# Kernel optimization log

Measured on AMD Instinct MI355X. Metric: run time of the kernel, lower is better.

## Reference

```python
import jax, jax.numpy as jnp
import numpy as np

N = 4096
DIN, DOUT, HID, CUTS = 16, 16, 16, 8
RADIUS = 9.0
SCALES = (1.0, 2.0, 3.0, 5.0, 10.0)
REG = 0.01
CHUNK = 512
GROUPS = 4
DINF = DIN + 2 * len(SCALES)  # 26


def leaky(v):
    return jnp.where(v >= 0, v, 0.2 * v)


def sqdist(a, b):
    d2 = jnp.sum(a * a, -1)[:, None] + jnp.sum(b * b, -1)[None, :] - 2.0 * (a @ b.T)
    return jnp.maximum(d2, 0.0)


def tangent_vectors(n):
    # Duff et al. branchless orthonormal basis, as in dMaSIF geometry_processing
    x, y, z = n[..., 0], n[..., 1], n[..., 2]
    s = jnp.where(z >= 0, 1.0, -1.0)
    a = -1.0 / (s + z)
    b = x * y * a
    t1 = jnp.stack([1.0 + s * x * x * a, s * b, -s * x], -1)
    t2 = jnp.stack([b, s + y * y * a, -y], -1)
    return jnp.stack([t1, t2], axis=-2)  # (..., 2, 3)


def group_norm(x, w, b, eps=1e-5):
    # torch GroupNorm(4, C) applied on (1, C, N): normalize over (C/G, N) per group
    n, c = x.shape
    xt = x.T.reshape(GROUPS, c // GROUPS, n)
    m = jnp.mean(xt, axis=(1, 2), keepdims=True)
    v = jnp.mean((xt - m) ** 2, axis=(1, 2), keepdims=True)
    xt = (xt - m) / jnp.sqrt(v + eps)
    return (xt.reshape(c, n) * w[:, None] + b[:, None]).T


def curvature_features(verts, normals):
    # dMaSIF curvatures(): per-scale Gaussian-window covariances, shape operator S = PPt^-1 PQt
    # Pairwise sums factorized into matmuls with the (N,N) window (no (N,N,8) intermediates).
    n_pts = verts.shape[0]
    d2 = sqdist(verts, verts)
    xx = (verts[:, :, None] * verts[:, None, :]).reshape(n_pts, 9)
    feats = []
    for s in SCALES:
        w = jnp.exp(-d2 / (2.0 * s * s))
        u_n = w @ normals  # scale-smoothed normals
        ns = u_n / jnp.maximum(jnp.linalg.norm(u_n, axis=-1, keepdims=True), 1e-12)
        uv = tangent_vectors(ns)  # (N,2,3)
        s0 = jnp.sum(w, 1)
        sx = w @ verts
        sn = w @ ns
        sxx = (w @ xx).reshape(n_pts, 3, 3)
        xn = (verts[:, :, None] * ns[:, None, :]).reshape(n_pts, 9)
        sxn = (w @ xn).reshape(n_pts, 3, 3)
        # sum_j w_ij (x_j-x_i)(x_j-x_i)^T  and  sum_j w_ij (x_j-x_i)(n_j-n_i)^T
        cxx = sxx - verts[:, :, None] * sx[:, None, :] - sx[:, :, None] * verts[:, None, :] \
              + s0[:, None, None] * verts[:, :, None] * verts[:, None, :]
        cxn = sxn - verts[:, :, None] * sn[:, None, :] - sx[:, :, None] * ns[:, None, :] \
              + s0[:, None, None] * verts[:, :, None] * ns[:, None, :]
        ppt = jnp.einsum('nka,nab,nlb->nkl', uv, cxx, uv) + REG * jnp.eye(2, dtype=verts.dtype)
        pqt = jnp.einsum('nka,nab,nlb->nkl', uv, cxn, uv)
        S = jnp.linalg.solve(ppt, pqt)  # (N,2,2)
        feats.append(jnp.clip(S[:, 0, 0] + S[:, 1, 1], -1.0, 1.0))            # mean curvature
        feats.append(jnp.clip(S[:, 0, 0] * S[:, 1, 1] - S[:, 0, 1] * S[:, 1, 0], -1.0, 1.0))  # gauss
    return jnp.stack(feats, -1)  # (N, 2*len(SCALES))


def _forward(verts, vnormals, x, os_w1, os_b1, os_w2, os_b2,
             ni_w1, ni_b1, ni_w2, ni_b2, gn_in_w, gn_in_b,
             cv_a1, cv_b1, cv_a2, cv_b2, no_w1, no_b1, no_w2, no_b2,
             gn_out_w, gn_out_b, ll_w1, ll_b1, ll_w2, ll_b2, lt_w, lt_b):
    curv = curvature_features(verts, vnormals)
    xf = jnp.concatenate([x, curv], axis=-1)  # (N, DINF)
    w = leaky(xf @ os_w1.T + os_b1) @ os_w2.T + os_b2  # orientation scores (N,1)

    # --- load_mesh: steer tangent frames along the gradient of w ---
    p = verts / RADIUS
    ndot = vnormals @ vnormals.T
    W = jnp.exp(-sqdist(p, p) * (2.0 - ndot) ** 2)  # pseudo-geodesic Gaussian window
    uv = tangent_vectors(vnormals)  # (N,2,3)
    ov3 = W @ (w * p) - (W @ w) * p  # sum_j W_ij w_j (x_j - x_i), factorized
    ov = jnp.einsum('nkd,nd->nk', uv, ov3) + 1e-5
    u = ov / jnp.sqrt(jnp.sum(ov * ov, -1, keepdims=True))
    ex, ey = u[:, 0:1], u[:, 1:2]
    u0, v0 = uv[:, 0], uv[:, 1]
    nuv = jnp.concatenate([vnormals[:, None, :],
                           (ex * u0 + ey * v0)[:, None, :],
                           (-ey * u0 + ex * v0)[:, None, :]], axis=1)  # (N,3,3)

    # --- dMaSIFConv layer ---
    h = leaky(leaky(xf @ ni_w1.T + ni_b1) @ ni_w2.T + ni_b2)
    h = group_norm(h, gn_in_w, gn_in_b)  # (N, HID)
    n_all = nuv[:, 0]
    nc = N // CHUNK
    pc = p.reshape(nc, CHUNK, 3)
    nuvc = nuv.reshape(nc, CHUNK, 3, 3)

    def block(args):
        pi, nuvi = args  # (C,3), (C,3,3)
        dx = p[None, :, :] - pi[:, None, :]  # (C,N,3)
        d2 = jnp.sum(dx * dx, -1)
        win = jnp.exp(-d2 * (2.0 - nuvi[:, 0] @ n_all.T) ** 2)  # (C,N)
        X = jnp.einsum('ckd,cnd->cnk', nuvi, dx)  # local coords (C,N,3)
        y = jax.nn.relu(X @ cv_a1.T + cv_b1) @ cv_a2.T + cv_b2  # filter MLP (C,N,HID)
        return jnp.einsum('cn,cnh,nh->ch', win, y, h)

    xi = jax.lax.map(jax.checkpoint(block), (pc, nuvc)).reshape(N, HID)
    xi = group_norm(leaky(leaky(xi @ no_w1.T + no_b1) @ no_w2.T + no_b2), gn_out_w, gn_out_b)
    xi = jax.nn.relu(xi @ ll_w1.T + ll_b1) @ ll_w2.T + ll_b2  # linear_layers[0]
    return xf @ lt_w.T + lt_b + xi  # linear_transform skip + conv branch


def setup_inputs():
    key = jax.random.key(0)
    ks = jax.random.split(key, 20)

    def lin(k, o, i):
        wk = jax.random.fold_in(k, 0)
        bk = jax.random.fold_in(k, 1)
        return ((1.0 / np.sqrt(i)) * jax.random.normal(wk, (o, i)),
                0.01 * jax.random.normal(bk, (o,)))

    verts = 10.0 * jax.random.normal(ks[0], (N, 3))
    vn = jax.random.normal(ks[1], (N, 3))
    vnormals = vn / jnp.linalg.norm(vn, axis=-1, keepdims=True)
    x = jax.random.normal(ks[2], (N, DIN))
    os_w1, os_b1 = lin(ks[3], DOUT, DINF)
    os_w2, os_b2 = lin(ks[4], 1, DOUT)
    ni_w1, ni_b1 = lin(ks[5], HID, DINF)
    ni_w2, ni_b2 = lin(ks[6], HID, HID)
    cv_a1 = jax.random.normal(ks[7], (CUTS, 3))
    cv_b1 = jax.random.uniform(ks[8], (CUTS,)) * 0.8 * jnp.sqrt(jnp.sum(cv_a1 ** 2, -1))
    cv_a2 = jax.random.uniform(ks[9], (HID, CUTS), minval=-1.0, maxval=1.0) / np.sqrt(CUTS)
    cv_b2 = jax.random.normal(ks[10], (HID,)) * 0.5 * jnp.sqrt(jnp.sum(cv_a2 ** 2, -1))
    no_w1, no_b1 = lin(ks[11], DOUT, HID)
    no_w2, no_b2 = lin(ks[12], DOUT, DOUT)
    ll_w1, ll_b1 = lin(ks[13], DOUT, DOUT)
    ll_w2, ll_b2 = lin(ks[14], DOUT, DOUT)
    lt_w, lt_b = lin(ks[15], DOUT, DINF)
    return {'verts': verts, 'vnormals': vnormals, 'x': x,
            'os_w1': os_w1, 'os_b1': os_b1, 'os_w2': os_w2, 'os_b2': os_b2,
            'ni_w1': ni_w1, 'ni_b1': ni_b1, 'ni_w2': ni_w2, 'ni_b2': ni_b2,
            'gn_in_w': jnp.ones(HID), 'gn_in_b': jnp.zeros(HID),
            'cv_a1': cv_a1, 'cv_b1': cv_b1, 'cv_a2': cv_a2, 'cv_b2': cv_b2,
            'no_w1': no_w1, 'no_b1': no_b1, 'no_w2': no_w2, 'no_b2': no_b2,
            'gn_out_w': jnp.ones(DOUT), 'gn_out_b': jnp.zeros(DOUT),
            'll_w1': ll_w1, 'll_b1': ll_b1, 'll_w2': ll_w2, 'll_b2': ll_b2,
            'lt_w': lt_w, 'lt_b': lt_b}


def reference(verts, vnormals, x, os_w1, os_b1, os_w2, os_b2,
              ni_w1, ni_b1, ni_w2, ni_b2, gn_in_w, gn_in_b,
              cv_a1, cv_b1, cv_a2, cv_b2, no_w1, no_b1, no_w2, no_b2,
              gn_out_w, gn_out_b, ll_w1, ll_b1, ll_w2, ll_b2, lt_w, lt_b):
    return _forward(verts, vnormals, x, os_w1, os_b1, os_w2, os_b2,
                    ni_w1, ni_b1, ni_w2, ni_b2, gn_in_w, gn_in_b,
                    cv_a1, cv_b1, cv_a2, cv_b2, no_w1, no_b1, no_w2, no_b2,
                    gn_out_w, gn_out_b, ll_w1, ll_b1, ll_w2, ll_b2, lt_w, lt_b)
```

## Files before the change

### kernel.cpp

```cpp
#include <hip/hip_runtime.h>
#include <hip/hip_bf16.h>
#include <math.h>

#define NPTS 4096
#define DINF 26
#define LOG2E 1.44269504088896f
#define JSPL 4

typedef float f32x4v __attribute__((ext_vector_type(4)));
typedef __bf16 bf16x8v __attribute__((ext_vector_type(8)));
typedef unsigned short ushort_t;

__device__ __forceinline__ float ldb(const float* p, int i){ return p[i]; }
__device__ __forceinline__ float lk(float v){ return v >= 0.0f ? v : 0.2f*v; }
__device__ __forceinline__ float wsum64(float v){
#pragma unroll
  for(int o=32;o>0;o>>=1) v += __shfl_down(v,o);
  return v;
}
__device__ __forceinline__ unsigned short f2bf(float f){
  return __builtin_bit_cast(unsigned short, __float2bfloat16(f));
}
__device__ __forceinline__ float bf2f(unsigned short u){
  return __bfloat162float(__builtin_bit_cast(__hip_bfloat16, u));
}
__device__ __forceinline__ void wave_lds_fence(){
  __builtin_amdgcn_wave_barrier();
  __builtin_amdgcn_s_waitcnt(0xC07F);
  __builtin_amdgcn_wave_barrier();
}
__device__ __forceinline__ void tangent(float nx,float ny,float nz,float* t1,float* t2){
  float s = (nz >= 0.0f) ? 1.0f : -1.0f;
  float a = -1.0f/(s+nz);
  float b = nx*ny*a;
  t1[0]=1.0f+s*nx*nx*a; t1[1]=s*b; t1[2]=-s*nx;
  t2[0]=b; t2[1]=s+ny*ny*a; t2[2]=-ny;
}

__global__ __launch_bounds__(256) void k0_convert(const float* __restrict__ verts,
                                                  const float* __restrict__ vnorm,
                                                  const float* __restrict__ x,
                                                  float* __restrict__ vertsF,
                                                  float* __restrict__ nF,
                                                  float* __restrict__ pF,
                                                  float* __restrict__ xfF){
  int i = blockIdx.x*blockDim.x + threadIdx.x;
  if(i >= NPTS) return;
#pragma unroll
  for(int d=0;d<3;d++){
    float v = verts[i*3+d];
    vertsF[i*3+d]=v;
    pF[i*3+d]=v*(1.0f/9.0f);
    nF[i*3+d]=vnorm[i*3+d];
  }
#pragma unroll
  for(int c=0;c<16;c++) xfF[i*DINF+c]=x[i*16+c];
}

__global__ __launch_bounds__(256) void kF(const float* __restrict__ vertsF,
                                          const float* __restrict__ nF,
                                          ushort_t* __restrict__ F1h,
                                          ushort_t* __restrict__ F1l){
  int j = blockIdx.x*256 + threadIdx.x;
  float vx=vertsF[j*3+0], vy=vertsF[j*3+1], vz=vertsF[j*3+2];
  float fv[16];
  fv[0]=1.0f; fv[1]=vx; fv[2]=vy; fv[3]=vz;
  fv[4]=vx*vx; fv[5]=vx*vy; fv[6]=vx*vz; fv[7]=vy*vy; fv[8]=vy*vz; fv[9]=vz*vz;
  fv[10]=nF[j*3+0]; fv[11]=nF[j*3+1]; fv[12]=nF[j*3+2];
  fv[13]=0.0f; fv[14]=0.0f; fv[15]=0.0f;
#pragma unroll
  for(int c=0;c<16;c++){
    unsigned short h=f2bf(fv[c]);
    F1h[c*NPTS+j]=h;
    F1l[c*NPTS+j]=f2bf(fv[c]-bf2f(h));
  }
}

__global__ __launch_bounds__(256) void k1m(const float* __restrict__ vertsF,
                                           const ushort_t* __restrict__ F1h,
                                           const ushort_t* __restrict__ F1l,
                                           float* __restrict__ sc){
  __shared__ __align__(16) float vq[4][64][4];
  __shared__ float red[4][16][16];
  const float c2e[5] = {0.5f*LOG2E, 0.125f*LOG2E, (1.0f/18.0f)*LOG2E,
                        0.02f*LOG2E, 0.005f*LOG2E};
  int lane = threadIdx.x & 63, w = threadIdx.x >> 6;
  int c16 = lane & 15, q = lane >> 4;
  int it = blockIdx.x >> 2, jseg = blockIdx.x & (JSPL-1);
  int i0 = it*16;
  int ia = i0 + c16;
  float vix=vertsF[ia*3+0], viy=vertsF[ia*3+1], viz=vertsF[ia*3+2];
  float nsqi = vix*vix+viy*viy+viz*viz;
  f32x4v acc[5];
#pragma unroll
  for(int s=0;s<5;s++) acc[s] = (f32x4v){0.0f,0.0f,0.0f,0.0f};

  int jbeg = jseg*(NPTS/JSPL) + w*(NPTS/JSPL/4);
  int jend = jbeg + (NPTS/JSPL/4);
#pragma unroll 1
  for(int jb=jbeg; jb<jend; jb+=64){
    int j = jb + lane;
    float vx=vertsF[j*3+0], vy=vertsF[j*3+1], vz=vertsF[j*3+2];
    *(float4*)&vq[w][lane][0] = make_float4(vx,vy,vz,vx*vx+vy*vy+vz*vz);
    wave_lds_fence();
#pragma unroll
    for(int q2=0;q2<2;q2++){
      int rb = q2*32 + q*8;
      bf16x8v bh = *(const bf16x8v*)(F1h + c16*NPTS + jb + rb);
      bf16x8v bl = *(const bf16x8v*)(F1l + c16*NPTS + jb + rb);
      bf16x8v af[5];
#pragma unroll
      for(int t=0;t<8;t++){
        float4 vv = *(const float4*)&vq[w][rb+t][0];
        float dot = vix*vv.x + viy*vv.y + viz*vv.z;
        float d2 = fmaxf(nsqi + vv.w - 2.0f*dot, 0.0f);
#pragma unroll
        for(int s=0;s<5;s++)
          af[s][t] = __builtin_bit_cast(__bf16, f2bf(exp2f(-d2*c2e[s])));
      }
#pragma unroll
      for(int s=0;s<5;s++){
        acc[s] = __builtin_amdgcn_mfma_f32_16x16x32_bf16(af[s], bh, acc[s], 0,0,0);
        acc[s] = __builtin_amdgcn_mfma_f32_16x16x32_bf16(af[s], bl, acc[s], 0,0,0);
      }
    }
    wave_lds_fence();
  }
#pragma unroll
  for(int s=0;s<5;s++){
#pragma unroll
    for(int r=0;r<4;r++) red[w][q*4+r][c16] = acc[s][r];
    __syncthreads();
    if(w==0){
      float* base = sc + (size_t)s*13*NPTS;
#pragma unroll
      for(int r=0;r<4;r++){
        int m = q*4+r, i = i0+m;
        float D = red[0][m][c16]+red[1][m][c16]+red[2][m][c16]+red[3][m][c16];
        if(c16==0)       atomicAdd(&base[i], D);
        else if(c16<4)   atomicAdd(&base[NPTS + i*3 + (c16-1)], D);
        else if(c16<10)  atomicAdd(&base[4*NPTS + i*6 + (c16-4)], D);
        else if(c16<13)  atomicAdd(&base[10*NPTS + i*3 + (c16-10)], D);
      }
    }
    __syncthreads();
  }
}

__global__ __launch_bounds__(256) void k2p(const float* __restrict__ vertsF,
                                           const float* __restrict__ sc,
                                           ushort_t* __restrict__ F2h,
                                           ushort_t* __restrict__ F2l){
  int idx = blockIdx.x*256 + threadIdx.x;
  int j = idx & (NPTS-1);
  int s = idx >> 12;
  float vx=vertsF[j*3+0], vy=vertsF[j*3+1], vz=vertsF[j*3+2];
  const float* ub = sc + (size_t)s*13*NPTS + 10*NPTS + (size_t)j*3;
  float ux=ub[0], uy=ub[1], uz=ub[2];
  float inv = 1.0f/fmaxf(sqrtf(ux*ux+uy*uy+uz*uz), 1e-12f);
  float n0=ux*inv, n1=uy*inv, n2=uz*inv;
  float fv[16];
  fv[0]=n0; fv[1]=n1; fv[2]=n2;
  fv[3]=vx*n0; fv[4]=vx*n1; fv[5]=vx*n2;
  fv[6]=vy*n0; fv[7]=vy*n1; fv[8]=vy*n2;
  fv[9]=vz*n0; fv[10]=vz*n1; fv[11]=vz*n2;
  fv[12]=0.0f; fv[13]=0.0f; fv[14]=0.0f; fv[15]=0.0f;
#pragma unroll
  for(int c=0;c<16;c++){
    unsigned short h=f2bf(fv[c]);
    F2h[((size_t)s*16+c)*NPTS+j]=h;
    F2l[((size_t)s*16+c)*NPTS+j]=f2bf(fv[c]-bf2f(h));
  }
}

__global__ __launch_bounds__(256) void k2m(const float* __restrict__ vertsF,
                                           const ushort_t* __restrict__ F2h,
                                           const ushort_t* __restrict__ F2l,
                                           float* __restrict__ mom2){
  __shared__ __align__(16) float vq[4][64][4];
  __shared__ float red[4][16][16];
  const float c2e[5] = {0.5f*LOG2E, 0.125f*LOG2E, (1.0f/18.0f)*LOG2E,
                        0.02f*LOG2E, 0.005f*LOG2E};
  int lane = threadIdx.x & 63, w = threadIdx.x >> 6;
  int c16 = lane & 15, q = lane >> 4;
  int it = blockIdx.x >> 2, jseg = blockIdx.x & (JSPL-1);
  int i0 = it*16;
  int ia = i0 + c16;
  float vix=vertsF[ia*3+0], viy=vertsF[ia*3+1], viz=vertsF[ia*3+2];
  float nsqi = vix*vix+viy*viy+viz*viz;
  f32x4v acc[5];
#pragma unroll
  for(int s=0;s<5;s++) acc[s] = (f32x4v){0.0f,0.0f,0.0f,0.0f};

  int jbeg = jseg*(NPTS/JSPL) + w*(NPTS/JSPL/4);
  int jend = jbeg + (NPTS/JSPL/4);
#pragma unroll 1
  for(int jb=jbeg; jb<jend; jb+=64){
    int j = jb + lane;
    float vx=vertsF[j*3+0], vy=vertsF[j*3+1], vz=vertsF[j*3+2];
    *(float4*)&vq[w][lane][0] = make_float4(vx,vy,vz,vx*vx+vy*vy+vz*vz);
    wave_lds_fence();
#pragma unroll
    for(int q2=0;q2<2;q2++){
      int rb = q2*32 + q*8;
      float d2t[8];
#pragma unroll
      for(int t=0;t<8;t++){
        float4 vv = *(const float4*)&vq[w][rb+t][0];
        float dot = vix*vv.x + viy*vv.y + viz*vv.z;
        d2t[t] = fmaxf(nsqi + vv.w - 2.0f*dot, 0.0f);
      }
#pragma unroll
      for(int s=0;s<5;s++){
        bf16x8v bh = *(const bf16x8v*)(F2h + ((size_t)s*16+c16)*NPTS + jb + rb);
        bf16x8v bl = *(const bf16x8v*)(F2l + ((size_t)s*16+c16)*NPTS + jb + rb);
        bf16x8v af;
#pragma unroll
        for(int t=0;t<8;t++)
          af[t] = __builtin_bit_cast(__bf16, f2bf(exp2f(-d2t[t]*c2e[s])));
        acc[s] = __builtin_amdgcn_mfma_f32_16x16x32_bf16(af, bh, acc[s], 0,0,0);
        acc[s] = __builtin_amdgcn_mfma_f32_16x16x32_bf16(af, bl, acc[s], 0,0,0);
      }
    }
    wave_lds_fence();
  }
#pragma unroll
  for(int s=0;s<5;s++){
#pragma unroll
    for(int r=0;r<4;r++) red[w][q*4+r][c16] = acc[s][r];
    __syncthreads();
    if(w==0){
#pragma unroll
      for(int r=0;r<4;r++){
        int m = q*4+r, i = i0+m;
        float D = red[0][m][c16]+red[1][m][c16]+red[2][m][c16]+red[3][m][c16];
        if(c16<12) atomicAdd(&mom2[((size_t)s*NPTS + i)*12 + c16], D);
      }
    }
    __syncthreads();
  }
}

__global__ __launch_bounds__(256) void k2s(const float* __restrict__ vertsF,
                                           const float* __restrict__ sc,
                                           const float* __restrict__ mom2,
                                           float* __restrict__ xfF){
  int idx = blockIdx.x*256 + threadIdx.x;
  int i = idx & (NPTS-1);
  int s = idx >> 12;
  const float* base = sc + (size_t)s*13*NPTS;
  float v[3] = { vertsF[i*3+0], vertsF[i*3+1], vertsF[i*3+2] };
  float s0 = base[i];
  float sx[3] = { base[NPTS+i*3+0], base[NPTS+i*3+1], base[NPTS+i*3+2] };
  float sxx6[6];
#pragma unroll
  for(int k=0;k<6;k++) sxx6[k]=base[4*NPTS+i*6+k];
  float ux=base[10*NPTS+i*3+0], uy=base[10*NPTS+i*3+1], uz=base[10*NPTS+i*3+2];
  float invn = 1.0f/fmaxf(sqrtf(ux*ux+uy*uy+uz*uz), 1e-12f);
  float nsi[3] = { ux*invn, uy*invn, uz*invn };
  const float* M2 = mom2 + ((size_t)s*NPTS + i)*12;
  float sn[3] = { M2[0], M2[1], M2[2] };
  float sxn[3][3];
#pragma unroll
  for(int a=0;a<3;a++)
#pragma unroll
    for(int b=0;b<3;b++) sxn[a][b]=M2[3+a*3+b];
  const int m6[3][3]={{0,1,2},{1,3,4},{2,4,5}};
  float cxx[3][3], cxn[3][3];
#pragma unroll
  for(int a=0;a<3;a++)
#pragma unroll
    for(int b=0;b<3;b++){
      cxx[a][b]=sxx6[m6[a][b]] - v[a]*sx[b] - sx[a]*v[b] + s0*v[a]*v[b];
      cxn[a][b]=sxn[a][b]    - v[a]*sn[b] - sx[a]*nsi[b] + s0*v[a]*nsi[b];
    }
  float t1[3],t2[3];
  tangent(nsi[0],nsi[1],nsi[2],t1,t2);
  float ppt[2][2], pqt[2][2];
#pragma unroll
  for(int k=0;k<2;k++){
    const float* tk = (k==0)?t1:t2;
#pragma unroll
    for(int l=0;l<2;l++){
      const float* tl = (l==0)?t1:t2;
      float accx=0.0f, accn=0.0f;
#pragma unroll
      for(int a=0;a<3;a++)
#pragma unroll
        for(int b=0;b<3;b++){
          accx += tk[a]*cxx[a][b]*tl[b];
          accn += tk[a]*cxn[a][b]*tl[b];
        }
      ppt[k][l]=accx + ((k==l)?0.01f:0.0f);
      pqt[k][l]=accn;
    }
  }
  float det = ppt[0][0]*ppt[1][1]-ppt[0][1]*ppt[1][0];
  float id = 1.0f/det;
  float S00=( ppt[1][1]*pqt[0][0]-ppt[0][1]*pqt[1][0])*id;
  float S01=( ppt[1][1]*pqt[0][1]-ppt[0][1]*pqt[1][1])*id;
  float S10=(-ppt[1][0]*pqt[0][0]+ppt[0][0]*pqt[1][0])*id;
  float S11=(-ppt[1][0]*pqt[0][1]+ppt[0][0]*pqt[1][1])*id;
  float f0=fminf(fmaxf(S00+S11,-1.0f),1.0f);
  float f1=fminf(fmaxf(S00*S11-S01*S10,-1.0f),1.0f);
  xfF[i*DINF+16+2*s]=f0;
  xfF[i*DINF+17+2*s]=f1;
}

__global__ __launch_bounds__(256) void k3_mlps(const float* __restrict__ xfF,
    const float* os_w1, const float* os_b1, const float* os_w2, const float* os_b2,
    const float* ni_w1, const float* ni_b1, const float* ni_w2, const float* ni_b2,
    float* __restrict__ wOS, float* __restrict__ hPre, float* __restrict__ stats){
  int i = blockIdx.x*256 + threadIdx.x;
  int lane = threadIdx.x & 63;
  float xf[DINF];
#pragma unroll
  for(int k=0;k<DINF;k++) xf[k]=xfF[i*DINF+k];
  float h1[16];
#pragma unroll
  for(int o=0;o<16;o++){
    float t=ldb(os_b1,o);
#pragma unroll
    for(int k=0;k<DINF;k++) t += xf[k]*ldb(os_w1,o*DINF+k);
    h1[o]=lk(t);
  }
  float w=ldb(os_b2,0);
#pragma unroll
  for(int o=0;o<16;o++) w += h1[o]*ldb(os_w2,o);
  wOS[i]=w;
#pragma unroll
  for(int o=0;o<16;o++){
    float t=ldb(ni_b1,o);
#pragma unroll
    for(int k=0;k<DINF;k++) t += xf[k]*ldb(ni_w1,o*DINF+k);
    h1[o]=lk(t);
  }
  float h2[16];
#pragma unroll
  for(int o=0;o<16;o++){
    float t=ldb(ni_b2,o);
#pragma unroll
    for(int k=0;k<16;k++) t += h1[k]*ldb(ni_w2,o*16+k);
    h2[o]=lk(t);
    hPre[i*16+o]=h2[o];
  }
  float gs[4]={0,0,0,0}, gq[4]={0,0,0,0};
#pragma unroll
  for(int c=0;c<16;c++){ gs[c>>2]+=h2[c]; gq[c>>2]+=h2[c]*h2[c]; }
  __shared__ float ls[8];
  if(threadIdx.x<8) ls[threadIdx.x]=0.0f;
  __syncthreads();
#pragma unroll
  for(int g=0;g<4;g++){ gs[g]=wsum64(gs[g]); gq[g]=wsum64(gq[g]); }
  if(lane==0){
#pragma unroll
    for(int g=0;g<4;g++){ atomicAdd(&ls[2*g],gs[g]); atomicAdd(&ls[2*g+1],gq[g]); }
  }
  __syncthreads();
  if(threadIdx.x<8) atomicAdd(&stats[threadIdx.x], ls[threadIdx.x]);
}

__global__ __launch_bounds__(256) void k3c_gn(const float* __restrict__ hPre,
                                              const float* __restrict__ stats,
                                              const float* gw, const float* gb,
                                              ushort_t* __restrict__ hTb){
  int i = blockIdx.x*256 + threadIdx.x;
  float m[4], r[4];
#pragma unroll
  for(int g=0;g<4;g++){
    float mean = stats[2*g]*(1.0f/(4.0f*NPTS));
    float var  = stats[2*g+1]*(1.0f/(4.0f*NPTS)) - mean*mean;
    m[g]=mean; r[g]=1.0f/sqrtf(var+1e-5f);
  }
#pragma unroll
  for(int c=0;c<16;c++){
    int g=c>>2;
    float v=(hPre[i*16+c]-m[g])*r[g]*ldb(gw,c)+ldb(gb,c);
    hTb[c*NPTS+i]=f2bf(v);
  }
}

__global__ __launch_bounds__(256) void kB(const float* __restrict__ pF,
                                          const float* __restrict__ wOS,
                                          ushort_t* __restrict__ B4h,
                                          ushort_t* __restrict__ B4l){
  int j = blockIdx.x*256 + threadIdx.x;
  float wj=wOS[j];
  float fv[16];
  fv[0]=wj*pF[j*3+0]; fv[1]=wj*pF[j*3+1]; fv[2]=wj*pF[j*3+2]; fv[3]=wj;
#pragma unroll
  for(int c=4;c<16;c++) fv[c]=0.0f;
#pragma unroll
  for(int c=0;c<16;c++){
    unsigned short h=f2bf(fv[c]);
    B4h[c*NPTS+j]=h;
    B4l[c*NPTS+j]=f2bf(fv[c]-bf2f(h));
  }
}

__global__ __launch_bounds__(512) void k4m(const float* __restrict__ pF,
                                           const float* __restrict__ nF,
                                           const ushort_t* __restrict__ B4h,
                                           const ushort_t* __restrict__ B4l,
                                           float* __restrict__ nuvF){
  __shared__ __align__(16) float vq[8][64][8];
  __shared__ float red[8][16][4];
  int lane = threadIdx.x & 63, w = threadIdx.x >> 6;
  int c16 = lane & 15, q = lane >> 4;
  int i0 = blockIdx.x*16;
  int ia = i0 + c16;
  float pix=pF[ia*3+0], piy=pF[ia*3+1], piz=pF[ia*3+2];
  float nix=nF[ia*3+0], niy=nF[ia*3+1], niz=nF[ia*3+2];
  f32x4v acc = {0.0f,0.0f,0.0f,0.0f};

#pragma unroll 1
  for(int jb=w*512; jb<w*512+512; jb+=64){
    int j = jb + lane;
    *(float4*)&vq[w][lane][0] = make_float4(pF[j*3+0],pF[j*3+1],pF[j*3+2],0.0f);
    *(float4*)&vq[w][lane][4] = make_float4(nF[j*3+0],nF[j*3+1],nF[j*3+2],0.0f);
    wave_lds_fence();
#pragma unroll
    for(int q2=0;q2<2;q2++){
      int rb = q2*32 + q*8;
      bf16x8v bh = *(const bf16x8v*)(B4h + c16*NPTS + jb + rb);
      bf16x8v bl = *(const bf16x8v*)(B4l + c16*NPTS + jb + rb);
      bf16x8v af;
#pragma unroll
      for(int t=0;t<8;t++){
        float4 P  = *(const float4*)&vq[w][rb+t][0];
        float4 Nj = *(const float4*)&vq[w][rb+t][4];
        float dx=P.x-pix, dy=P.y-piy, dz=P.z-piz;
        float d2=dx*dx+dy*dy+dz*dz;
        float f=2.0f-(Nj.x*nix+Nj.y*niy+Nj.z*niz);
        af[t]=__builtin_bit_cast(__bf16, f2bf(exp2f(-d2*f*f*LOG2E)));
      }
      acc = __builtin_amdgcn_mfma_f32_16x16x32_bf16(af, bh, acc, 0,0,0);
      acc = __builtin_amdgcn_mfma_f32_16x16x32_bf16(af, bl, acc, 0,0,0);
    }
    wave_lds_fence();
  }
#pragma unroll
  for(int r=0;r<4;r++) if(c16<4) red[w][q*4+r][c16]=acc[r];
  __syncthreads();
  if(threadIdx.x<16){
    int tid=threadIdx.x, i=i0+tid;
    float a0=0,a1=0,a2=0,a3=0;
#pragma unroll
    for(int ww=0;ww<8;ww++){
      a0+=red[ww][tid][0]; a1+=red[ww][tid][1];
      a2+=red[ww][tid][2]; a3+=red[ww][tid][3];
    }
    float pix2=pF[i*3+0], piy2=pF[i*3+1], piz2=pF[i*3+2];
    float nix2=nF[i*3+0], niy2=nF[i*3+1], niz2=nF[i*3+2];
    float o0=a0-a3*pix2, o1=a1-a3*piy2, o2=a2-a3*piz2;
    float t1[3],t2[3];
    tangent(nix2,niy2,niz2,t1,t2);
    float ov0=t1[0]*o0+t1[1]*o1+t1[2]*o2+1e-5f;
    float ov1=t2[0]*o0+t2[1]*o1+t2[2]*o2+1e-5f;
    float inv=1.0f/sqrtf(ov0*ov0+ov1*ov1);
    float ex=ov0*inv, ey=ov1*inv;
    nuvF[i*9+0]=nix2; nuvF[i*9+1]=niy2; nuvF[i*9+2]=niz2;
    nuvF[i*9+3]= ex*t1[0]+ey*t2[0]; nuvF[i*9+4]= ex*t1[1]+ey*t2[1]; nuvF[i*9+5]= ex*t1[2]+ey*t2[2];
    nuvF[i*9+6]=-ey*t1[0]+ex*t2[0]; nuvF[i*9+7]=-ey*t1[1]+ex*t2[1]; nuvF[i*9+8]=-ey*t1[2]+ex*t2[2];
  }
}

__global__ __launch_bounds__(256) void k5_conv(const float* __restrict__ pF,
                                               const float* __restrict__ nF,
                                               const float* __restrict__ nuvF,
                                               const ushort_t* __restrict__ hTb,
                                               const float* cv_a1, const float* cv_b1,
                                               const float* cv_a2, const float* cv_b2,
                                               float* __restrict__ xiP){
  __shared__ __align__(16) float vq[4][64][8];
  __shared__ float red[4][64][4];
  int lane = threadIdx.x & 63, w = threadIdx.x >> 6;
  int c16 = lane & 15, q = lane >> 4;
  int it = blockIdx.x >> 2, jseg = blockIdx.x & (JSPL-1);
  int i0 = it*16;
  int i = i0 + c16;
  float pix=pF[i*3+0], piy=pF[i*3+1], piz=pF[i*3+2];
  float nu[9];
#pragma unroll
  for(int k=0;k<9;k++) nu[k]=nuvF[i*9+k];
  float a1w[8][3], b1w[8];
#pragma unroll
  for(int c=0;c<8;c++){
    a1w[c][0]=cv_a1[c*3+0]; a1w[c][1]=cv_a1[c*3+1]; a1w[c][2]=cv_a1[c*3+2];
    b1w[c]=cv_b1[c];
  }
  f32x4v acc[9];
#pragma unroll
  for(int c=0;c<9;c++) acc[c]=(f32x4v){0.0f,0.0f,0.0f,0.0f};

  int jbeg = jseg*(NPTS/JSPL) + w*(NPTS/JSPL/4);
  int jend = jbeg + (NPTS/JSPL/4);
#pragma unroll 1
  for(int jb=jbeg; jb<jend; jb+=64){
    int j = jb + lane;
    *(float4*)&vq[w][lane][0] = make_float4(pF[j*3+0],pF[j*3+1],pF[j*3+2],0.0f);
    *(float4*)&vq[w][lane][4] = make_float4(nF[j*3+0],nF[j*3+1],nF[j*3+2],0.0f);
    wave_lds_fence();
#pragma unroll
    for(int q2=0;q2<2;q2++){
      int jb2 = jb + q2*32;
      bf16x8v bfr = *(const bf16x8v*)(hTb + c16*NPTS + jb2 + q*8);
      bf16x8v af[9];
#pragma unroll
      for(int t=0;t<8;t++){
        int rloc = q2*32 + q*8 + t;
        float4 P  = *(const float4*)&vq[w][rloc][0];
        float4 Nj = *(const float4*)&vq[w][rloc][4];
        float dx=P.x-pix, dy=P.y-piy, dz=P.z-piz;
        float d2=dx*dx+dy*dy+dz*dz;
        float f=2.0f-(Nj.x*nu[0]+Nj.y*nu[1]+Nj.z*nu[2]);
        float win=exp2f(-d2*f*f*LOG2E);
        float X0=nu[0]*dx+nu[1]*dy+nu[2]*dz;
        float X1=nu[3]*dx+nu[4]*dy+nu[5]*dz;
        float X2=nu[6]*dx+nu[7]*dy+nu[8]*dz;
#pragma unroll
        for(int c=0;c<8;c++){
          float r=fmaf(X0,a1w[c][0],fmaf(X1,a1w[c][1],fmaf(X2,a1w[c][2],b1w[c])));
          af[c][t]=__builtin_bit_cast(__bf16, f2bf(win*fmaxf(r,0.0f)));
        }
        af[8][t]=__builtin_bit_cast(__bf16, f2bf(win));
      }
#pragma unroll
      for(int c=0;c<9;c++)
        acc[c] = __builtin_amdgcn_mfma_f32_16x16x32_bf16(af[c], bfr, acc[c], 0,0,0);
    }
    wave_lds_fence();
  }
  float a2row[8];
#pragma unroll
  for(int c=0;c<8;c++) a2row[c]=cv_a2[c16*8+c];
  float b2v = cv_b2[c16];
#pragma unroll
  for(int r=0;r<4;r++){
    float xi = acc[8][r]*b2v;
#pragma unroll
    for(int c=0;c<8;c++) xi += acc[c][r]*a2row[c];
    red[w][lane][r]=xi;
  }
  __syncthreads();
  if(w==0){
#pragma unroll
    for(int r=0;r<4;r++){
      float v = red[0][lane][r]+red[1][lane][r]+red[2][lane][r]+red[3][lane][r];
      xiP[((size_t)jseg*NPTS + (i0 + q*4 + r))*16 + c16] = v;
    }
  }
}

__global__ __launch_bounds__(256) void k6a(const float* __restrict__ xiP,
    const float* no_w1, const float* no_b1, const float* no_w2, const float* no_b2,
    float* __restrict__ tF, float* __restrict__ stats2){
  int i = blockIdx.x*256 + threadIdx.x;
  int lane = threadIdx.x & 63;
  float xi[16];
#pragma unroll
  for(int k=0;k<16;k++){
    float v=0.0f;
#pragma unroll
    for(int s=0;s<JSPL;s++) v += xiP[((size_t)s*NPTS + i)*16 + k];
    xi[k]=v;
  }
  float t1[16];
#pragma unroll
  for(int o=0;o<16;o++){
    float t=ldb(no_b1,o);
#pragma unroll
    for(int k=0;k<16;k++) t += xi[k]*ldb(no_w1,o*16+k);
    t1[o]=lk(t);
  }
  float t2[16];
#pragma unroll
  for(int o=0;o<16;o++){
    float t=ldb(no_b2,o);
#pragma unroll
    for(int k=0;k<16;k++) t += t1[k]*ldb(no_w2,o*16+k);
    t2[o]=lk(t);
    tF[i*16+o]=t2[o];
  }
  float gs[4]={0,0,0,0}, gq[4]={0,0,0,0};
#pragma unroll
  for(int c=0;c<16;c++){ gs[c>>2]+=t2[c]; gq[c>>2]+=t2[c]*t2[c]; }
  __shared__ float ls[8];
  if(threadIdx.x<8) ls[threadIdx.x]=0.0f;
  __syncthreads();
#pragma unroll
  for(int g=0;g<4;g++){ gs[g]=wsum64(gs[g]); gq[g]=wsum64(gq[g]); }
  if(lane==0){
#pragma unroll
    for(int g=0;g<4;g++){ atomicAdd(&ls[2*g],gs[g]); atomicAdd(&ls[2*g+1],gq[g]); }
  }
  __syncthreads();
  if(threadIdx.x<8) atomicAdd(&stats2[threadIdx.x], ls[threadIdx.x]);
}

__global__ __launch_bounds__(256) void k6c(const float* __restrict__ tF,
    const float* __restrict__ xfF, const float* __restrict__ stats2,
    const float* gw, const float* gb,
    const float* ll_w1, const float* ll_b1, const float* ll_w2, const float* ll_b2,
    const float* lt_w, const float* lt_b,
    float* __restrict__ out){
  int i = blockIdx.x*256 + threadIdx.x;
  float m[4], r[4];
#pragma unroll
  for(int g=0;g<4;g++){
    float mean = stats2[2*g]*(1.0f/(4.0f*NPTS));
    float var  = stats2[2*g+1]*(1.0f/(4.0f*NPTS)) - mean*mean;
    m[g]=mean; r[g]=1.0f/sqrtf(var+1e-5f);
  }
  float tn[16];
#pragma unroll
  for(int c=0;c<16;c++){
    int g=c>>2;
    tn[c]=(tF[i*16+c]-m[g])*r[g]*ldb(gw,c)+ldb(gb,c);
  }
  float z1[16];
#pragma unroll
  for(int o=0;o<16;o++){
    float t=ldb(ll_b1,o);
#pragma unroll
    for(int k=0;k<16;k++) t += tn[k]*ldb(ll_w1,o*16+k);
    z1[o]=fmaxf(t,0.0f);
  }
  float xf[DINF];
#pragma unroll
  for(int k=0;k<DINF;k++) xf[k]=xfF[i*DINF+k];
#pragma unroll
  for(int o=0;o<16;o++){
    float z=ldb(ll_b2,o);
#pragma unroll
    for(int k=0;k<16;k++) z += z1[k]*ldb(ll_w2,o*16+k);
    float lt=ldb(lt_b,o);
#pragma unroll
    for(int k=0;k<DINF;k++) lt += xf[k]*ldb(lt_w,o*DINF+k);
    out[i*16+o]=z+lt;
  }
}

extern "C" void kernel_launch(void* const* d_in, const int* in_sizes, int n_in,
                              void* d_out, int out_size, void* d_ws, size_t ws_size,
                              hipStream_t stream){
  const float* verts    = (const float*)d_in[0];
  const float* vnormals = (const float*)d_in[1];
  const float* x        = (const float*)d_in[2];
  const float* os_w1    = (const float*)d_in[3];
  const float* os_b1    = (const float*)d_in[4];
  const float* os_w2    = (const float*)d_in[5];
  const float* os_b2    = (const float*)d_in[6];
  const float* ni_w1    = (const float*)d_in[7];
  const float* ni_b1    = (const float*)d_in[8];
  const float* ni_w2    = (const float*)d_in[9];
  const float* ni_b2    = (const float*)d_in[10];
  const float* gn_in_w  = (const float*)d_in[11];
  const float* gn_in_b  = (const float*)d_in[12];
  const float* cv_a1    = (const float*)d_in[13];
  const float* cv_b1    = (const float*)d_in[14];
  const float* cv_a2    = (const float*)d_in[15];
  const float* cv_b2    = (const float*)d_in[16];
  const float* no_w1    = (const float*)d_in[17];
  const float* no_b1    = (const float*)d_in[18];
  const float* no_w2    = (const float*)d_in[19];
  const float* no_b2    = (const float*)d_in[20];
  const float* gn_out_w = (const float*)d_in[21];
  const float* gn_out_b = (const float*)d_in[22];
  const float* ll_w1    = (const float*)d_in[23];
  const float* ll_b1    = (const float*)d_in[24];
  const float* ll_w2    = (const float*)d_in[25];
  const float* ll_b2    = (const float*)d_in[26];
  const float* lt_w     = (const float*)d_in[27];
  const float* lt_b     = (const float*)d_in[28];

  float* W = (float*)d_ws;
  size_t off = 0;
  float* vertsF = W + off; off += (size_t)3*NPTS;
  float* nF     = W + off; off += (size_t)3*NPTS;
  float* pF     = W + off; off += (size_t)3*NPTS;
  float* xfF    = W + off; off += (size_t)DINF*NPTS;
  float* sc     = W + off; off += (size_t)13*NPTS*5;
  float* wOS    = W + off; off += (size_t)NPTS;
  float* hPre   = W + off; off += (size_t)16*NPTS;
  ushort_t* hTb = (ushort_t*)(W + off); off += (size_t)8*NPTS;
  float* nuvF   = W + off; off += (size_t)9*NPTS;
  float* xiP    = W + off; off += (size_t)JSPL*16*NPTS;
  float* tF     = W + off; off += (size_t)16*NPTS;
  float* stats  = W + off; off += 16;
  ushort_t* F1h = (ushort_t*)(W + off); off += (size_t)8*NPTS;
  ushort_t* F1l = (ushort_t*)(W + off); off += (size_t)8*NPTS;
  ushort_t* F2h = (ushort_t*)(W + off); off += (size_t)40*NPTS;
  ushort_t* F2l = (ushort_t*)(W + off); off += (size_t)40*NPTS;
  ushort_t* B4h = (ushort_t*)(W + off); off += (size_t)8*NPTS;
  ushort_t* B4l = (ushort_t*)(W + off); off += (size_t)8*NPTS;
  float* mom2 = hPre;

  hipMemsetAsync(stats, 0, 16*sizeof(float), stream);
  hipMemsetAsync(sc,   0, (size_t)13*NPTS*5*sizeof(float), stream);
  hipMemsetAsync(mom2, 0, (size_t)12*NPTS*5*sizeof(float), stream);

  k0_convert<<<NPTS/256, 256, 0, stream>>>(verts, vnormals, x, vertsF, nF, pF, xfF);
  kF<<<NPTS/256, 256, 0, stream>>>(vertsF, nF, F1h, F1l);
  k1m<<<(NPTS/16)*JSPL, 256, 0, stream>>>(vertsF, F1h, F1l, sc);
  k2p<<<5*NPTS/256, 256, 0, stream>>>(vertsF, sc, F2h, F2l);
  k2m<<<(NPTS/16)*JSPL, 256, 0, stream>>>(vertsF, F2h, F2l, mom2);
  k2s<<<5*NPTS/256, 256, 0, stream>>>(vertsF, sc, mom2, xfF);
  k3_mlps<<<NPTS/256, 256, 0, stream>>>(xfF, os_w1, os_b1, os_w2, os_b2,
                                        ni_w1, ni_b1, ni_w2, ni_b2, wOS, hPre, stats);
  k3c_gn<<<NPTS/256, 256, 0, stream>>>(hPre, stats, gn_in_w, gn_in_b, hTb);
  kB<<<NPTS/256, 256, 0, stream>>>(pF, wOS, B4h, B4l);
  k4m<<<NPTS/16, 512, 0, stream>>>(pF, nF, B4h, B4l, nuvF);
  k5_conv<<<(NPTS/16)*JSPL, 256, 0, stream>>>(pF, nF, nuvF, hTb,
                                              cv_a1, cv_b1, cv_a2, cv_b2, xiP);
  k6a<<<NPTS/256, 256, 0, stream>>>(xiP, no_w1, no_b1, no_w2, no_b2, tF, stats+8);
  k6c<<<NPTS/256, 256, 0, stream>>>(tF, xfF, stats+8, gn_out_w, gn_out_b,
                                    ll_w1, ll_b1, ll_w2, ll_b2, lt_w, lt_b, (float*)d_out);
}
```

Baseline: 310.7 us.

## Fuse small elementwise kernels, merge memsets, and tile k2m over two row blocks

Folds kF into k0_convert, k2s into k3_mlps (as k23), and kB into k3c_gn. This removes three launches and the intermediate global round-trips between them. The three memsets become one contiguous memset by moving sc, mom2 and stats next to each other, so mom2 no longer aliases hPre. k2m now handles 32 rows per block with 8 column splits, so each loaded F2 fragment feeds twice as many MFMAs, at the cost of more registers and more exp work per wave.

```diff
diff --git a/kernel.cpp b/kernel.cpp
--- a/kernel.cpp
+++ b/kernel.cpp
@@ -6,6 +6,7 @@
 #define DINF 26
 #define LOG2E 1.44269504088896f
 #define JSPL 4
+#define JS2  8
 
 typedef float f32x4v __attribute__((ext_vector_type(4)));
 typedef __bf16 bf16x8v __attribute__((ext_vector_type(8)));
@@ -43,37 +44,28 @@
                                                   float* __restrict__ vertsF,
                                                   float* __restrict__ nF,
                                                   float* __restrict__ pF,
-                                                  float* __restrict__ xfF){
+                                                  float* __restrict__ xfF,
+                                                  ushort_t* __restrict__ F1h,
+                                                  ushort_t* __restrict__ F1l){
   int i = blockIdx.x*blockDim.x + threadIdx.x;
   if(i >= NPTS) return;
-#pragma unroll
-  for(int d=0;d<3;d++){
-    float v = verts[i*3+d];
-    vertsF[i*3+d]=v;
-    pF[i*3+d]=v*(1.0f/9.0f);
-    nF[i*3+d]=vnorm[i*3+d];
-  }
-#pragma unroll
-  for(int c=0;c<16;c++) xfF[i*DINF+c]=x[i*16+c];
-}
-
-__global__ __launch_bounds__(256) void kF(const float* __restrict__ vertsF,
-                                          const float* __restrict__ nF,
-                                          ushort_t* __restrict__ F1h,
-                                          ushort_t* __restrict__ F1l){
-  int j = blockIdx.x*256 + threadIdx.x;
-  float vx=vertsF[j*3+0], vy=vertsF[j*3+1], vz=vertsF[j*3+2];
+  float vx=verts[i*3+0], vy=verts[i*3+1], vz=verts[i*3+2];
+  float nx=vnorm[i*3+0], ny=vnorm[i*3+1], nz=vnorm[i*3+2];
+  vertsF[i*3+0]=vx; vertsF[i*3+1]=vy; vertsF[i*3+2]=vz;
+  nF[i*3+0]=nx; nF[i*3+1]=ny; nF[i*3+2]=nz;
+  pF[i*3+0]=vx*(1.0f/9.0f); pF[i*3+1]=vy*(1.0f/9.0f); pF[i*3+2]=vz*(1.0f/9.0f);
   float fv[16];
   fv[0]=1.0f; fv[1]=vx; fv[2]=vy; fv[3]=vz;
   fv[4]=vx*vx; fv[5]=vx*vy; fv[6]=vx*vz; fv[7]=vy*vy; fv[8]=vy*vz; fv[9]=vz*vz;
-  fv[10]=nF[j*3+0]; fv[11]=nF[j*3+1]; fv[12]=nF[j*3+2];
-  fv[13]=0.0f; fv[14]=0.0f; fv[15]=0.0f;
+  fv[10]=nx; fv[11]=ny; fv[12]=nz; fv[13]=0.0f; fv[14]=0.0f; fv[15]=0.0f;
 #pragma unroll
   for(int c=0;c<16;c++){
     unsigned short h=f2bf(fv[c]);
-    F1h[c*NPTS+j]=h;
-    F1l[c*NPTS+j]=f2bf(fv[c]-bf2f(h));
-  }
+    F1h[c*NPTS+i]=h;
+    F1l[c*NPTS+i]=f2bf(fv[c]-bf2f(h));
+  }
+#pragma unroll
+  for(int c=0;c<16;c++) xfF[i*DINF+c]=x[i*16+c];
 }
 
 __global__ __launch_bounds__(256) void k1m(const float* __restrict__ vertsF,
@@ -105,13 +97,13 @@
     wave_lds_fence();
 #pragma unroll
     for(int q2=0;q2<2;q2++){
-      int rb = q2*32 + q*8;
-      bf16x8v bh = *(const bf16x8v*)(F1h + c16*NPTS + jb + rb);
-      bf16x8v bl = *(const bf16x8v*)(F1l + c16*NPTS + jb + rb);
+      int rb = jb + q2*32 + q*8;
+      bf16x8v bh = *(const bf16x8v*)(F1h + c16*NPTS + rb);
+      bf16x8v bl = *(const bf16x8v*)(F1l + c16*NPTS + rb);
       bf16x8v af[5];
 #pragma unroll
       for(int t=0;t<8;t++){
-        float4 vv = *(const float4*)&vq[w][rb+t][0];
+        float4 vv = *(const float4*)&vq[w][q2*32+q*8+t][0];
         float dot = vix*vv.x + viy*vv.y + viz*vv.z;
         float d2 = fmaxf(nsqi + vv.w - 2.0f*dot, 0.0f);
 #pragma unroll
@@ -183,17 +175,21 @@
                         0.02f*LOG2E, 0.005f*LOG2E};
   int lane = threadIdx.x & 63, w = threadIdx.x >> 6;
   int c16 = lane & 15, q = lane >> 4;
-  int it = blockIdx.x >> 2, jseg = blockIdx.x & (JSPL-1);
-  int i0 = it*16;
-  int ia = i0 + c16;
-  float vix=vertsF[ia*3+0], viy=vertsF[ia*3+1], viz=vertsF[ia*3+2];
-  float nsqi = vix*vix+viy*viy+viz*viz;
-  f32x4v acc[5];
-#pragma unroll
-  for(int s=0;s<5;s++) acc[s] = (f32x4v){0.0f,0.0f,0.0f,0.0f};
-
-  int jbeg = jseg*(NPTS/JSPL) + w*(NPTS/JSPL/4);
-  int jend = jbeg + (NPTS/JSPL/4);
+  int it = blockIdx.x >> 3, jseg = blockIdx.x & (JS2-1);
+  int iA = it*32 + c16, iB = iA + 16;
+  float vax=vertsF[iA*3+0], vay=vertsF[iA*3+1], vaz=vertsF[iA*3+2];
+  float nsqA = vax*vax+vay*vay+vaz*vaz;
+  float vbx=vertsF[iB*3+0], vby=vertsF[iB*3+1], vbz=vertsF[iB*3+2];
+  float nsqB = vbx*vbx+vby*vby+vbz*vbz;
+  f32x4v accA[5], accB[5];
+#pragma unroll
+  for(int s=0;s<5;s++){
+    accA[s] = (f32x4v){0.0f,0.0f,0.0f,0.0f};
+    accB[s] = (f32x4v){0.0f,0.0f,0.0f,0.0f};
+  }
+
+  int jbeg = jseg*(NPTS/JS2) + w*(NPTS/JS2/4);
+  int jend = jbeg + (NPTS/JS2/4);
 #pragma unroll 1
   for(int jb=jbeg; jb<jend; jb+=64){
     int j = jb + lane;
@@ -202,112 +198,58 @@
     wave_lds_fence();
 #pragma unroll
     for(int q2=0;q2<2;q2++){
-      int rb = q2*32 + q*8;
-      float d2t[8];
+      int rb = jb + q2*32 + q*8;
+      float d2A[8], d2B[8];
 #pragma unroll
       for(int t=0;t<8;t++){
-        float4 vv = *(const float4*)&vq[w][rb+t][0];
-        float dot = vix*vv.x + viy*vv.y + viz*vv.z;
-        d2t[t] = fmaxf(nsqi + vv.w - 2.0f*dot, 0.0f);
+        float4 vv = *(const float4*)&vq[w][q2*32+q*8+t][0];
+        float dotA = vax*vv.x + vay*vv.y + vaz*vv.z;
+        float dotB = vbx*vv.x + vby*vv.y + vbz*vv.z;
+        d2A[t] = fmaxf(nsqA + vv.w - 2.0f*dotA, 0.0f);
+        d2B[t] = fmaxf(nsqB + vv.w - 2.0f*dotB, 0.0f);
       }
 #pragma unroll
       for(int s=0;s<5;s++){
-        bf16x8v bh = *(const bf16x8v*)(F2h + ((size_t)s*16+c16)*NPTS + jb + rb);
-        bf16x8v bl = *(const bf16x8v*)(F2l + ((size_t)s*16+c16)*NPTS + jb + rb);
-        bf16x8v af;
-#pragma unroll
-        for(int t=0;t<8;t++)
-          af[t] = __builtin_bit_cast(__bf16, f2bf(exp2f(-d2t[t]*c2e[s])));
-        acc[s] = __builtin_amdgcn_mfma_f32_16x16x32_bf16(af, bh, acc[s], 0,0,0);
-        acc[s] = __builtin_amdgcn_mfma_f32_16x16x32_bf16(af, bl, acc[s], 0,0,0);
+        bf16x8v bh = *(const bf16x8v*)(F2h + ((size_t)s*16+c16)*NPTS + rb);
+        bf16x8v bl = *(const bf16x8v*)(F2l + ((size_t)s*16+c16)*NPTS + rb);
+        bf16x8v afA, afB;
+#pragma unroll
+        for(int t=0;t<8;t++){
+          afA[t] = __builtin_bit_cast(__bf16, f2bf(exp2f(-d2A[t]*c2e[s])));
+          afB[t] = __builtin_bit_cast(__bf16, f2bf(exp2f(-d2B[t]*c2e[s])));
+        }
+        accA[s] = __builtin_amdgcn_mfma_f32_16x16x32_bf16(afA, bh, accA[s], 0,0,0);
+        accA[s] = __builtin_amdgcn_mfma_f32_16x16x32_bf16(afA, bl, accA[s], 0,0,0);
+        accB[s] = __builtin_amdgcn_mfma_f32_16x16x32_bf16(afB, bh, accB[s], 0,0,0);
+        accB[s] = __builtin_amdgcn_mfma_f32_16x16x32_bf16(afB, bl, accB[s], 0,0,0);
       }
     }
     wave_lds_fence();
   }
 #pragma unroll
-  for(int s=0;s<5;s++){
-#pragma unroll
-    for(int r=0;r<4;r++) red[w][q*4+r][c16] = acc[s][r];
-    __syncthreads();
-    if(w==0){
-#pragma unroll
-      for(int r=0;r<4;r++){
-        int m = q*4+r, i = i0+m;
-        float D = red[0][m][c16]+red[1][m][c16]+red[2][m][c16]+red[3][m][c16];
-        if(c16<12) atomicAdd(&mom2[((size_t)s*NPTS + i)*12 + c16], D);
-      }
-    }
-    __syncthreads();
-  }
-}
-
-__global__ __launch_bounds__(256) void k2s(const float* __restrict__ vertsF,
-                                           const float* __restrict__ sc,
-                                           const float* __restrict__ mom2,
-                                           float* __restrict__ xfF){
-  int idx = blockIdx.x*256 + threadIdx.x;
-  int i = idx & (NPTS-1);
-  int s = idx >> 12;
-  const float* base = sc + (size_t)s*13*NPTS;
-  float v[3] = { vertsF[i*3+0], vertsF[i*3+1], vertsF[i*3+2] };
-  float s0 = base[i];
-  float sx[3] = { base[NPTS+i*3+0], base[NPTS+i*3+1], base[NPTS+i*3+2] };
-  float sxx6[6];
-#pragma unroll
-  for(int k=0;k<6;k++) sxx6[k]=base[4*NPTS+i*6+k];
-  float ux=base[10*NPTS+i*3+0], uy=base[10*NPTS+i*3+1], uz=base[10*NPTS+i*3+2];
-  float invn = 1.0f/fmaxf(sqrtf(ux*ux+uy*uy+uz*uz), 1e-12f);
-  float nsi[3] = { ux*invn, uy*invn, uz*invn };
-  const float* M2 = mom2 + ((size_t)s*NPTS + i)*12;
-  float sn[3] = { M2[0], M2[1], M2[2] };
-  float sxn[3][3];
-#pragma unroll
-  for(int a=0;a<3;a++)
-#pragma unroll
-    for(int b=0;b<3;b++) sxn[a][b]=M2[3+a*3+b];
-  const int m6[3][3]={{0,1,2},{1,3,4},{2,4,5}};
-  float cxx[3][3], cxn[3][3];
-#pragma unroll
-  for(int a=0;a<3;a++)
-#pragma unroll
-    for(int b=0;b<3;b++){
-      cxx[a][b]=sxx6[m6[a][b]] - v[a]*sx[b] - sx[a]*v[b] + s0*v[a]*v[b];
-      cxn[a][b]=sxn[a][b]    - v[a]*sn[b] - sx[a]*nsi[b] + s0*v[a]*nsi[b];
-    }
-  float t1[3],t2[3];
-  tangent(nsi[0],nsi[1],nsi[2],t1,t2);
-  float ppt[2][2], pqt[2][2];
-#pragma unroll
-  for(int k=0;k<2;k++){
-    const float* tk = (k==0)?t1:t2;
-#pragma unroll
-    for(int l=0;l<2;l++){
-      const float* tl = (l==0)?t1:t2;
-      float accx=0.0f, accn=0.0f;
-#pragma unroll
-      for(int a=0;a<3;a++)
-#pragma unroll
-        for(int b=0;b<3;b++){
-          accx += tk[a]*cxx[a][b]*tl[b];
-          accn += tk[a]*cxn[a][b]*tl[b];
+  for(int sub=0; sub<2; sub++){
+    int ibase = it*32 + sub*16;
+#pragma unroll
+    for(int s=0;s<5;s++){
+#pragma unroll
+      for(int r=0;r<4;r++) red[w][q*4+r][c16] = (sub ? accB[s][r] : accA[s][r]);
+      __syncthreads();
+      if(w==0){
+#pragma unroll
+        for(int r=0;r<4;r++){
+          int m = q*4+r, i = ibase+m;
+          float D = red[0][m][c16]+red[1][m][c16]+red[2][m][c16]+red[3][m][c16];
+          if(c16<12) atomicAdd(&mom2[((size_t)s*NPTS + i)*12 + c16], D);
         }
-      ppt[k][l]=accx + ((k==l)?0.01f:0.0f);
-      pqt[k][l]=accn;
-    }
-  }
-  float det = ppt[0][0]*ppt[1][1]-ppt[0][1]*ppt[1][0];
-  float id = 1.0f/det;
-  float S00=( ppt[1][1]*pqt[0][0]-ppt[0][1]*pqt[1][0])*id;
-  float S01=( ppt[1][1]*pqt[0][1]-ppt[0][1]*pqt[1][1])*id;
-  float S10=(-ppt[1][0]*pqt[0][0]+ppt[0][0]*pqt[1][0])*id;
-  float S11=(-ppt[1][0]*pqt[0][1]+ppt[0][0]*pqt[1][1])*id;
-  float f0=fminf(fmaxf(S00+S11,-1.0f),1.0f);
-  float f1=fminf(fmaxf(S00*S11-S01*S10,-1.0f),1.0f);
-  xfF[i*DINF+16+2*s]=f0;
-  xfF[i*DINF+17+2*s]=f1;
-}
-
-__global__ __launch_bounds__(256) void k3_mlps(const float* __restrict__ xfF,
+      }
+      __syncthreads();
+    }
+  }
+}
+
+__global__ __launch_bounds__(256) void k23(const float* __restrict__ vertsF,
+    const float* __restrict__ sc, const float* __restrict__ mom2,
+    float* __restrict__ xfF,
     const float* os_w1, const float* os_b1, const float* os_w2, const float* os_b2,
     const float* ni_w1, const float* ni_b1, const float* ni_w2, const float* ni_b2,
     float* __restrict__ wOS, float* __restrict__ hPre, float* __restrict__ stats){
@@ -315,7 +257,68 @@
   int lane = threadIdx.x & 63;
   float xf[DINF];
 #pragma unroll
-  for(int k=0;k<DINF;k++) xf[k]=xfF[i*DINF+k];
+  for(int k=0;k<16;k++) xf[k]=xfF[i*DINF+k];
+  float v[3] = { vertsF[i*3+0], vertsF[i*3+1], vertsF[i*3+2] };
+#pragma unroll 1
+  for(int s=0;s<5;s++){
+    const float* base = sc + (size_t)s*13*NPTS;
+    float s0 = base[i];
+    float sx[3] = { base[NPTS+i*3+0], base[NPTS+i*3+1], base[NPTS+i*3+2] };
+    float sxx6[6];
+#pragma unroll
+    for(int k=0;k<6;k++) sxx6[k]=base[4*NPTS+i*6+k];
+    float ux=base[10*NPTS+i*3+0], uy=base[10*NPTS+i*3+1], uz=base[10*NPTS+i*3+2];
+    float invn = 1.0f/fmaxf(sqrtf(ux*ux+uy*uy+uz*uz), 1e-12f);
+    float nsi[3] = { ux*invn, uy*invn, uz*invn };
+    const float* M2 = mom2 + ((size_t)s*NPTS + i)*12;
+    float sn[3] = { M2[0], M2[1], M2[2] };
+    float sxn[3][3];
+#pragma unroll
+    for(int a=0;a<3;a++)
+#pragma unroll
+      for(int b=0;b<3;b++) sxn[a][b]=M2[3+a*3+b];
+    const int m6[3][3]={{0,1,2},{1,3,4},{2,4,5}};
+    float cxx[3][3], cxn[3][3];
+#pragma unroll
+    for(int a=0;a<3;a++)
+#pragma unroll
+      for(int b=0;b<3;b++){
+        cxx[a][b]=sxx6[m6[a][b]] - v[a]*sx[b] - sx[a]*v[b] + s0*v[a]*v[b];
+        cxn[a][b]=sxn[a][b]    - v[a]*sn[b] - sx[a]*nsi[b] + s0*v[a]*nsi[b];
+      }
+    float t1[3],t2[3];
+    tangent(nsi[0],nsi[1],nsi[2],t1,t2);
+    float ppt[2][2], pqt[2][2];
+#pragma unroll
+    for(int k=0;k<2;k++){
+      const float* tk = (k==0)?t1:t2;
+#pragma unroll
+      for(int l=0;l<2;l++){
+        const float* tl = (l==0)?t1:t2;
+        float accx=0.0f, accn=0.0f;
+#pragma unroll
+        for(int a=0;a<3;a++)
+#pragma unroll
+          for(int b=0;b<3;b++){
+            accx += tk[a]*cxx[a][b]*tl[b];
+            accn += tk[a]*cxn[a][b]*tl[b];
+          }
+        ppt[k][l]=accx + ((k==l)?0.01f:0.0f);
+        pqt[k][l]=accn;
+      }
+    }
+    float det = ppt[0][0]*ppt[1][1]-ppt[0][1]*ppt[1][0];
+    float id = 1.0f/det;
+    float S00=( ppt[1][1]*pqt[0][0]-ppt[0][1]*pqt[1][0])*id;
+    float S01=( ppt[1][1]*pqt[0][1]-ppt[0][1]*pqt[1][1])*id;
+    float S10=(-ppt[1][0]*pqt[0][0]+ppt[0][0]*pqt[1][0])*id;
+    float S11=(-ppt[1][0]*pqt[0][1]+ppt[0][0]*pqt[1][1])*id;
+    float f0=fminf(fmaxf(S00+S11,-1.0f),1.0f);
+    float f1=fminf(fmaxf(S00*S11-S01*S10,-1.0f),1.0f);
+    xf[16+2*s]=f0; xf[17+2*s]=f1;
+    xfF[i*DINF+16+2*s]=f0;
+    xfF[i*DINF+17+2*s]=f1;
+  }
   float h1[16];
 #pragma unroll
   for(int o=0;o<16;o++){
@@ -363,7 +366,11 @@
 __global__ __launch_bounds__(256) void k3c_gn(const float* __restrict__ hPre,
                                               const float* __restrict__ stats,
                                               const float* gw, const float* gb,
-                                              ushort_t* __restrict__ hTb){
+                                              const float* __restrict__ pF,
+                                              const float* __restrict__ wOS,
+                                              ushort_t* __restrict__ hTb,
+                                              ushort_t* __restrict__ B4h,
+                                              ushort_t* __restrict__ B4l){
   int i = blockIdx.x*256 + threadIdx.x;
   float m[4], r[4];
 #pragma unroll
@@ -378,23 +385,16 @@
     float v=(hPre[i*16+c]-m[g])*r[g]*ldb(gw,c)+ldb(gb,c);
     hTb[c*NPTS+i]=f2bf(v);
   }
-}
-
-__global__ __launch_bounds__(256) void kB(const float* __restrict__ pF,
-                                          const float* __restrict__ wOS,
-                                          ushort_t* __restrict__ B4h,
-                                          ushort_t* __restrict__ B4l){
-  int j = blockIdx.x*256 + threadIdx.x;
-  float wj=wOS[j];
+  float wj=wOS[i];
   float fv[16];
-  fv[0]=wj*pF[j*3+0]; fv[1]=wj*pF[j*3+1]; fv[2]=wj*pF[j*3+2]; fv[3]=wj;
+  fv[0]=wj*pF[i*3+0]; fv[1]=wj*pF[i*3+1]; fv[2]=wj*pF[i*3+2]; fv[3]=wj;
 #pragma unroll
   for(int c=4;c<16;c++) fv[c]=0.0f;
 #pragma unroll
   for(int c=0;c<16;c++){
     unsigned short h=f2bf(fv[c]);
-    B4h[c*NPTS+j]=h;
-    B4l[c*NPTS+j]=f2bf(fv[c]-bf2f(h));
+    B4h[c*NPTS+i]=h;
+    B4l[c*NPTS+i]=f2bf(fv[c]-bf2f(h));
   }
 }
 
@@ -421,14 +421,14 @@
     wave_lds_fence();
 #pragma unroll
     for(int q2=0;q2<2;q2++){
-      int rb = q2*32 + q*8;
-      bf16x8v bh = *(const bf16x8v*)(B4h + c16*NPTS + jb + rb);
-      bf16x8v bl = *(const bf16x8v*)(B4l + c16*NPTS + jb + rb);
+      int rb = jb + q2*32 + q*8;
+      bf16x8v bh = *(const bf16x8v*)(B4h + c16*NPTS + rb);
+      bf16x8v bl = *(const bf16x8v*)(B4l + c16*NPTS + rb);
       bf16x8v af;
 #pragma unroll
       for(int t=0;t<8;t++){
-        float4 P  = *(const float4*)&vq[w][rb+t][0];
-        float4 Nj = *(const float4*)&vq[w][rb+t][4];
+        float4 P  = *(const float4*)&vq[w][q2*32+q*8+t][0];
+        float4 Nj = *(const float4*)&vq[w][q2*32+q*8+t][4];
         float dx=P.x-pix, dy=P.y-piy, dz=P.z-piz;
         float d2=dx*dx+dy*dy+dz*dz;
         float f=2.0f-(Nj.x*nix+Nj.y*niy+Nj.z*niz);
@@ -503,8 +503,8 @@
     wave_lds_fence();
 #pragma unroll
     for(int q2=0;q2<2;q2++){
-      int jb2 = jb + q2*32;
-      bf16x8v bfr = *(const bf16x8v*)(hTb + c16*NPTS + jb2 + q*8);
+      int rb = jb + q2*32 + q*8;
+      bf16x8v bfr = *(const bf16x8v*)(hTb + c16*NPTS + rb);
       bf16x8v af[9];
 #pragma unroll
       for(int t=0;t<8;t++){
@@ -680,36 +680,36 @@
   float* nF     = W + off; off += (size_t)3*NPTS;
   float* pF     = W + off; off += (size_t)3*NPTS;
   float* xfF    = W + off; off += (size_t)DINF*NPTS;
-  float* sc     = W + off; off += (size_t)13*NPTS*5;
   float* wOS    = W + off; off += (size_t)NPTS;
   float* hPre   = W + off; off += (size_t)16*NPTS;
   ushort_t* hTb = (ushort_t*)(W + off); off += (size_t)8*NPTS;
   float* nuvF   = W + off; off += (size_t)9*NPTS;
   float* xiP    = W + off; off += (size_t)JSPL*16*NPTS;
   float* tF     = W + off; off += (size_t)16*NPTS;
-  float* stats  = W + off; off += 16;
   ushort_t* F1h = (ushort_t*)(W + off); off += (size_t)8*NPTS;
   ushort_t* F1l = (ushort_t*)(W + off); off += (size_t)8*NPTS;
   ushort_t* F2h = (ushort_t*)(W + off); off += (size_t)40*NPTS;
   ushort_t* F2l = (ushort_t*)(W + off); off += (size_t)40*NPTS;
   ushort_t* B4h = (ushort_t*)(W + off); off += (size_t)8*NPTS;
   ushort_t* B4l = (ushort_t*)(W + off); off += (size_t)8*NPTS;
-  float* mom2 = hPre;
-
-  hipMemsetAsync(stats, 0, 16*sizeof(float), stream);
-  hipMemsetAsync(sc,   0, (size_t)13*NPTS*5*sizeof(float), stream);
-  hipMemsetAsync(mom2, 0, (size_t)12*NPTS*5*sizeof(float), stream);
-
-  k0_convert<<<NPTS/256, 256, 0, stream>>>(verts, vnormals, x, vertsF, nF, pF, xfF);
-  kF<<<NPTS/256, 256, 0, stream>>>(vertsF, nF, F1h, F1l);
+  float* zr     = W + off;
+  float* sc     = W + off; off += (size_t)13*NPTS*5;
+  float* mom2   = W + off; off += (size_t)12*NPTS*5;
+  float* stats  = W + off; off += 16;
+  size_t zbytes = ((size_t)13*NPTS*5 + (size_t)12*NPTS*5 + 16)*sizeof(float);
+
+  hipMemsetAsync(zr, 0, zbytes, stream);
+
+  k0_convert<<<NPTS/256, 256, 0, stream>>>(verts, vnormals, x, vertsF, nF, pF, xfF,
+                                           F1h, F1l);
   k1m<<<(NPTS/16)*JSPL, 256, 0, stream>>>(vertsF, F1h, F1l, sc);
   k2p<<<5*NPTS/256, 256, 0, stream>>>(vertsF, sc, F2h, F2l);
-  k2m<<<(NPTS/16)*JSPL, 256, 0, stream>>>(vertsF, F2h, F2l, mom2);
-  k2s<<<5*NPTS/256, 256, 0, stream>>>(vertsF, sc, mom2, xfF);
-  k3_mlps<<<NPTS/256, 256, 0, stream>>>(xfF, os_w1, os_b1, os_w2, os_b2,
-                                        ni_w1, ni_b1, ni_w2, ni_b2, wOS, hPre, stats);
-  k3c_gn<<<NPTS/256, 256, 0, stream>>>(hPre, stats, gn_in_w, gn_in_b, hTb);
-  kB<<<NPTS/256, 256, 0, stream>>>(pF, wOS, B4h, B4l);
+  k2m<<<(NPTS/32)*JS2, 256, 0, stream>>>(vertsF, F2h, F2l, mom2);
+  k23<<<NPTS/256, 256, 0, stream>>>(vertsF, sc, mom2, xfF,
+                                    os_w1, os_b1, os_w2, os_b2,
+                                    ni_w1, ni_b1, ni_w2, ni_b2, wOS, hPre, stats);
+  k3c_gn<<<NPTS/256, 256, 0, stream>>>(hPre, stats, gn_in_w, gn_in_b,
+                                       pF, wOS, hTb, B4h, B4l);
   k4m<<<NPTS/16, 512, 0, stream>>>(pF, nF, B4h, B4l, nuvF);
   k5_conv<<<(NPTS/16)*JSPL, 256, 0, stream>>>(pF, nF, nuvF, hTb,
                                               cv_a1, cv_b1, cv_a2, cv_b2, xiP);
```

New measurement: 296.8 us. 1.05x faster.
